# Kernel tuning notes

Hardware: AMD Instinct MI355X
Metric: run time of the kernel (lower is better)

The kernel has to match this reference:

```python
import jax, jax.numpy as jnp
import numpy as np

B, S, D, H, HH, L = 256, 512, 128, 256, 128, 64
PATH_V, SYS_V = 10000, 500

def _gru_cell(gi_t, h, Whh, bhh):
    # PyTorch GRU cell: gi_t = x @ Wih.T + bih precomputed
    gh = h @ Whh.T + bhh
    ir, iz, inn = jnp.split(gi_t, 3, axis=-1)
    hr, hz, hn = jnp.split(gh, 3, axis=-1)
    r = jax.nn.sigmoid(ir + hr)
    z = jax.nn.sigmoid(iz + hz)
    n = jnp.tanh(inn + r * hn)
    return (1.0 - z) * n + z * h

def _gru_seq(x, Wih, Whh, bih, bhh):
    # x: [B,S,in] -> outputs [B,S,H], zero initial hidden (torch default)
    gi = jnp.einsum('bsd,hd->bsh', x, Wih) + bih  # precompute input gates once
    h0 = jnp.zeros((x.shape[0], Whh.shape[1]), x.dtype)
    def step(h, gi_t):
        hn = _gru_cell(gi_t, h, Whh, bhh)
        return hn, hn
    _, ys = jax.lax.scan(step, h0, jnp.swapaxes(gi, 0, 1))
    return jnp.swapaxes(ys, 0, 1)

def setup_inputs() -> dict:
    key = jax.random.key(0)
    ks = jax.random.split(key, 24)
    r = lambda k, shape: (jax.random.normal(k, shape, dtype=jnp.float32) * 0.05)
    inp = {
        'tokens': jax.random.randint(ks[0], (B, S, 2), 0, SYS_V, dtype=jnp.int64),
        'path_emb_w': r(ks[1], (PATH_V, D)),
        'sys_emb_w': r(ks[2], (SYS_V, D)),
        # encoder gru1: D -> H
        'e1_Wih': r(ks[3], (3 * H, D)), 'e1_Whh': r(ks[4], (3 * H, H)),
        'e1_bih': r(ks[5], (3 * H,)), 'e1_bhh': r(ks[6], (3 * H,)),
        # encoder gru2: H -> HH
        'e2_Wih': r(ks[7], (3 * HH, H)), 'e2_Whh': r(ks[8], (3 * HH, HH)),
        'e2_bih': r(ks[9], (3 * HH,)), 'e2_bhh': r(ks[10], (3 * HH,)),
        # linear1: HH -> L
        'l1_W': r(ks[11], (L, HH)), 'l1_b': r(ks[12], (L,)),
        # decoder gru1: L -> HH
        'd1_Wih': r(ks[13], (3 * HH, L)), 'd1_Whh': r(ks[14], (3 * HH, HH)),
        'd1_bih': r(ks[15], (3 * HH,)), 'd1_bhh': r(ks[16], (3 * HH,)),
        # decoder gru2: HH -> H
        'd2_Wih': r(ks[17], (3 * H, HH)), 'd2_Whh': r(ks[18], (3 * H, H)),
        'd2_bih': r(ks[19], (3 * H,)), 'd2_bhh': r(ks[20], (3 * H,)),
        # linear2: H -> D
        'l2_W': r(ks[21], (D, H)), 'l2_b': r(ks[22], (D,)),
    }
    return inp

def reference(tokens, path_emb_w, sys_emb_w,
              e1_Wih, e1_Whh, e1_bih, e1_bhh,
              e2_Wih, e2_Whh, e2_bih, e2_bhh,
              l1_W, l1_b,
              d1_Wih, d1_Whh, d1_bih, d1_bhh,
              d2_Wih, d2_Whh, d2_bih, d2_bhh,
              l2_W, l2_b):
    # embedding sum -> [B,S,D]
    emb = path_emb_w[tokens[:, :, 0]] + sys_emb_w[tokens[:, :, 1]]
    # encoder (dropout is identity at eval)
    h1_seq = _gru_seq(emb, e1_Wih, e1_Whh, e1_bih, e1_bhh)      # [B,S,H]
    h2_seq = _gru_seq(h1_seq, e2_Wih, e2_Whh, e2_bih, e2_bhh)    # [B,S,HH]
    latent = h2_seq[:, -1, :] @ l1_W.T + l1_b                    # [B,L]
    gi1 = latent @ d1_Wih.T + d1_bih                             # constant [B,3*HH]
    h10 = jnp.zeros((latent.shape[0], HH), latent.dtype)
    h20 = jnp.zeros((latent.shape[0], H), latent.dtype)
    def dec_step(carry, _):
        h1, h2 = carry
        h1 = _gru_cell(gi1, h1, d1_Whh, d1_bhh)
        gi2 = h1 @ d2_Wih.T + d2_bih
        h2 = _gru_cell(gi2, h2, d2_Whh, d2_bhh)
        out = h2 @ l2_W.T + l2_b                                 # linear2 per step
        return (h1, h2), out
    _, outs = jax.lax.scan(dec_step, (h10, h20), None, length=S)  # [S,B,D]
    recon = jnp.swapaxes(outs, 0, 1)                             # [B,S,D]
    recon_loss = jnp.mean((recon - emb) ** 2)
    return latent, recon_loss
```

## Files before the change

### kernel.cpp

```cpp
#include <hip/hip_runtime.h>
#include <cstddef>

typedef unsigned short u16;
typedef __bf16 bf16x8 __attribute__((ext_vector_type(8)));
typedef float f32x4 __attribute__((ext_vector_type(4)));
typedef unsigned short us4 __attribute__((ext_vector_type(4)));

__device__ __forceinline__ u16 f2b(float f) {
    unsigned u = __float_as_uint(f);
    u += 0x7fffu + ((u >> 16) & 1u);
    return (u16)(u >> 16);
}
__device__ __forceinline__ float b2f(u16 h) { return __uint_as_float(((unsigned)h) << 16); }

__device__ __forceinline__ f32x4 mfma16(bf16x8 a, bf16x8 b, f32x4 c) {
    return __builtin_amdgcn_mfma_f32_16x16x32_bf16(a, b, c, 0, 0, 0);
}

__device__ __forceinline__ void bar_lds() {
    asm volatile("s_waitcnt lgkmcnt(0)\n\ts_barrier" ::: "memory");
}

#define CH   64
#define NCH  8
#define MCH  (CH * 256)

struct PackSeg { const float* src; u16* dst; int K; int nfrag; };
struct PackArgs { PackSeg seg[8]; };

__global__ __launch_bounds__(64) void pack_all(PackArgs pa) {
    int f = blockIdx.x;
    int i = 0;
    while (i < 7 && f >= pa.seg[i].nfrag) { f -= pa.seg[i].nfrag; i++; }
    const float* W = pa.seg[i].src;
    u16* out = pa.seg[i].dst;
    int K = pa.seg[i].K;
    int lane = threadIdx.x, q = lane >> 4, ln = lane & 15;
    int KT = K >> 5;
    int nt = f / KT, kt = f % KT;
    int n = nt * 16 + ln;
    int kb = kt * 32 + q * 8;
#pragma unroll
    for (int j = 0; j < 8; j++)
        out[((size_t)f * 64 + lane) * 8 + j] = f2b(W[(size_t)n * K + kb + j]);
}

__global__ void zero_kernel(float* __restrict__ st, float* __restrict__ lossslot) {
    int i = blockIdx.x * 256 + threadIdx.x;
    if (i < 196608) st[i] = 0.f;
    if (i == 0) *lossslot = 0.f;
}

__global__ __launch_bounds__(256) void embed_kernel(const int* __restrict__ tok,
                                                    const float* __restrict__ pw,
                                                    const float* __restrict__ sw,
                                                    u16* __restrict__ emb) {
    int col = threadIdx.x & 127;
    int half = threadIdx.x >> 7;
    int rbase = blockIdx.x * 16;
#pragma unroll
    for (int i = 0; i < 8; i++) {
        int r = rbase + i * 2 + half;
        int b = r & 255, t = r >> 8;
        const int* tp = tok + ((size_t)b * 512 + t) * 2;
        float v = pw[(size_t)tp[0] * 128 + col] + sw[(size_t)tp[1] * 128 + col];
        emb[(size_t)r * 128 + col] = f2b(v);
    }
}

template <int K, int N>
__device__ __forceinline__ void gemm_body(int bid, char* ldsraw,
                                          const u16* __restrict__ X,
                                          const u16* __restrict__ Wp,
                                          const float* __restrict__ bias,
                                          const float* __restrict__ bhh,
                                          u16* __restrict__ out) {
    constexpr int NH = N / 2, KT = K / 32, NTL = NH / 16;
    u16* wl = (u16*)ldsraw;
    int tid = threadIdx.x, wid = tid >> 6, lane = tid & 63, q = lane >> 4, ln = lane & 15;
    int half = bid & 1, mg = bid >> 1;
    {
        const bf16x8* src = (const bf16x8*)(Wp + (size_t)half * NH * K);
        bf16x8* dst = (bf16x8*)wl;
#pragma unroll
        for (int i = 0; i < NH * K / 8 / 512; i++) dst[tid + i * 512] = src[tid + i * 512];
    }
    __syncthreads();
    int m0 = (mg * 8 + wid) * 16;
    int t = m0 >> 8, bg = (m0 >> 4) & 15;
    u16* obase = out + (size_t)(t * 16 + bg) * N * 16;
    bf16x8 af[KT];
#pragma unroll
    for (int kt = 0; kt < KT; kt++)
        af[kt] = *(const bf16x8*)(X + (size_t)(m0 + ln) * K + kt * 32 + q * 8);
    for (int nt = 0; nt < NTL; nt++) {
        f32x4 acc = {0.f, 0.f, 0.f, 0.f};
#pragma unroll
        for (int kt = 0; kt < KT; kt++)
            acc = mfma16(af[kt], *(const bf16x8*)&wl[((nt * KT + kt) * 64 + lane) * 8], acc);
        int g = half * NH + nt * 16 + ln;
        float bv = bias[g] + ((g < 2 * (N / 3)) ? bhh[g] : 0.f);
        us4 v;
#pragma unroll
        for (int r = 0; r < 4; r++) v[r] = f2b(acc[r] + bv);
        *(us4*)&obase[(size_t)g * 16 + 4 * q] = v;
    }
}

template <int K, int N>
__global__ __launch_bounds__(512, 2) void gemm_kernel(const u16* __restrict__ X,
                                                      const u16* __restrict__ Wp,
                                                      const float* __restrict__ bias,
                                                      const float* __restrict__ bhh,
                                                      u16* __restrict__ out) {
    __shared__ char lds[98304];
    gemm_body<K, N>(blockIdx.x, lds, X, Wp, bias, bhh, out);
}

__device__ __forceinline__ void loss_body(int bid, char* ldsraw,
                                          const u16* __restrict__ h2d,
                                          const u16* __restrict__ Wp,
                                          const float* __restrict__ l2b,
                                          const u16* __restrict__ embc,
                                          float* __restrict__ loss) {
    float* red = (float*)ldsraw;
    int tid = threadIdx.x, wid = tid >> 6, lane = tid & 63, q = lane >> 4, ln = lane & 15;
    int m0 = (bid * 8 + wid) * 16;
    bf16x8 af[8];
#pragma unroll
    for (int kt = 0; kt < 8; kt++)
        af[kt] = *(const bf16x8*)(h2d + (size_t)(m0 + ln) * 256 + kt * 32 + q * 8);
    float ls = 0.f;
#pragma unroll
    for (int nt = 0; nt < 8; nt++) {
        f32x4 acc = {0.f, 0.f, 0.f, 0.f};
#pragma unroll
        for (int kt = 0; kt < 8; kt++)
            acc = mfma16(af[kt], *(const bf16x8*)(Wp + ((size_t)(nt * 8 + kt) * 64 + lane) * 8), acc);
        int g = nt * 16 + ln;
        float bv = l2b[g];
#pragma unroll
        for (int r = 0; r < 4; r++) {
            float rec = acc[r] + bv;
            float ev = b2f(embc[(size_t)(m0 + q * 4 + r) * 128 + g]);
            float d = rec - ev;
            ls += d * d;
        }
    }
    red[tid] = ls;
    __syncthreads();
    for (int s = 256; s > 0; s >>= 1) {
        if (tid < s) red[tid] += red[tid + s];
        __syncthreads();
    }
    if (tid == 0) atomicAdd(loss, red[0] * (1.f / 16777216.f));
}

template <int H, bool GI_CONST, bool WRITE_SEQ>
__device__ __forceinline__ void rec_body(int bid, char* ldsraw,
                                         const u16* __restrict__ giT,
                                         const float* __restrict__ gic,
                                         const u16* __restrict__ Wp,
                                         const float* __restrict__ bhh,
                                         float* __restrict__ hstate,
                                         u16* __restrict__ hseq, int steps) {
    constexpr int G3 = 3 * H;
    constexpr int KT = H / 32;
    constexpr int NHF = H / 128;
    constexpr int HP = H + 8;
    constexpr bool WLDS = (H == 256);
    u16* wl = (u16*)ldsraw;
    u16 (*hl)[16][HP] = (u16 (*)[16][HP])(ldsraw + (WLDS ? 65536 : 0));

    const int tid = threadIdx.x, w = tid >> 6, lane = tid & 63, q = lane >> 4, ln = lane & 15;
    const int b0 = bid * 16;
    const bf16x8* wpv = (const bf16x8*)Wp;

    bf16x8 wfr[3][NHF][KT];
#pragma unroll
    for (int g = 0; g < 3; g++)
#pragma unroll
        for (int hh = 0; hh < NHF; hh++) {
            if (WLDS && g == 2 && hh == NHF - 1) continue;
#pragma unroll
            for (int kt = 0; kt < KT; kt++)
                wfr[g][hh][kt] = wpv[((size_t)(g * (H / 16) + NHF * w + hh) * KT + kt) * 64 + lane];
        }
    if (WLDS) {
#pragma unroll
        for (int kt = 0; kt < KT; kt++)
            *(bf16x8*)&wl[((w * KT + kt) * 64 + lane) * 8] =
                wpv[((size_t)(2 * (H / 16) + NHF * w + (NHF - 1)) * KT + kt) * 64 + lane];
    }
    float bhn_r[NHF];
#pragma unroll
    for (int hh = 0; hh < NHF; hh++) bhn_r[hh] = bhh[2 * H + 16 * (NHF * w + hh) + ln];

    float hold[NHF][4];
#pragma unroll
    for (int hh = 0; hh < NHF; hh++)
#pragma unroll
        for (int rg = 0; rg < 4; rg++) {
            const int b = 4 * q + rg, k = 16 * (NHF * w + hh) + ln;
            u16 hb = f2b(hstate[(size_t)(b0 + b) * H + k]);
            hold[hh][rg] = b2f(hb);
            hl[0][b][k] = hb;
        }

    float gcf[3][NHF][4];
    us4 gp[3][NHF];
    if (GI_CONST) {
#pragma unroll
        for (int g = 0; g < 3; g++)
#pragma unroll
            for (int hh = 0; hh < NHF; hh++)
#pragma unroll
                for (int rg = 0; rg < 4; rg++)
                    gcf[g][hh][rg] =
                        gic[(size_t)(b0 + 4 * q + rg) * G3 + g * H + 16 * (NHF * w + hh) + ln];
    } else {
        const u16* blk = giT + (size_t)bid * G3 * 16;
#pragma unroll
        for (int g = 0; g < 3; g++)
#pragma unroll
            for (int hh = 0; hh < NHF; hh++)
                gp[g][hh] = *(const us4*)&blk[(g * H + 16 * (NHF * w + hh) + ln) * 16 + 4 * q];
    }
    bar_lds();

    for (int t = 0; t < steps; t++) {
        const int p = t & 1;
        float gf2[NHF][4];
        f32x4 acc[3][NHF];
#pragma unroll
        for (int hh = 0; hh < NHF; hh++) {
#pragma unroll
            for (int rg = 0; rg < 4; rg++) {
                if (GI_CONST) {
                    acc[0][hh][rg] = gcf[0][hh][rg];
                    acc[1][hh][rg] = gcf[1][hh][rg];
                    gf2[hh][rg] = gcf[2][hh][rg];
                } else {
                    acc[0][hh][rg] = b2f(gp[0][hh][rg]);
                    acc[1][hh][rg] = b2f(gp[1][hh][rg]);
                    gf2[hh][rg] = b2f(gp[2][hh][rg]);
                }
                acc[2][hh][rg] = bhn_r[hh];
            }
        }
        if (!GI_CONST) {
            const int tn = (t + 1 < steps) ? t + 1 : t;
            const u16* blk = giT + (size_t)(tn * 16 + bid) * G3 * 16;
#pragma unroll
            for (int g = 0; g < 3; g++)
#pragma unroll
                for (int hh = 0; hh < NHF; hh++)
                    gp[g][hh] = *(const us4*)&blk[(g * H + 16 * (NHF * w + hh) + ln) * 16 + 4 * q];
        }

        u16* hsb = WRITE_SEQ ? (hseq + ((size_t)t * 256 + b0) * H) : nullptr;

#pragma unroll
        for (int hh = 0; hh < NHF; hh++) {
            const int k = 16 * (NHF * w + hh) + ln;
#pragma unroll
            for (int kh = 0; kh < KT / 2; kh++) {
                bf16x8 a0 = *(const bf16x8*)&hl[p][ln][(2 * kh) * 32 + q * 8];
                bf16x8 a1 = *(const bf16x8*)&hl[p][ln][(2 * kh + 1) * 32 + q * 8];
                acc[0][hh] = mfma16(a0, wfr[0][hh][2 * kh], acc[0][hh]);
                acc[0][hh] = mfma16(a1, wfr[0][hh][2 * kh + 1], acc[0][hh]);
                acc[1][hh] = mfma16(a0, wfr[1][hh][2 * kh], acc[1][hh]);
                acc[1][hh] = mfma16(a1, wfr[1][hh][2 * kh + 1], acc[1][hh]);
                if (WLDS && hh == NHF - 1) {
                    bf16x8 w0 = *(const bf16x8*)&wl[((w * KT + 2 * kh) * 64 + lane) * 8];
                    bf16x8 w1 = *(const bf16x8*)&wl[((w * KT + 2 * kh + 1) * 64 + lane) * 8];
                    acc[2][hh] = mfma16(a0, w0, acc[2][hh]);
                    acc[2][hh] = mfma16(a1, w1, acc[2][hh]);
                } else {
                    acc[2][hh] = mfma16(a0, wfr[2][hh][2 * kh], acc[2][hh]);
                    acc[2][hh] = mfma16(a1, wfr[2][hh][2 * kh + 1], acc[2][hh]);
                }
            }
#pragma unroll
            for (int rg = 0; rg < 4; rg++) {
                float xr = acc[0][hh][rg];
                float xz = acc[1][hh][rg];
                float hn = acc[2][hh][rg];
                float r = __builtin_amdgcn_rcpf(1.f + __builtin_amdgcn_exp2f(-1.44269504f * xr));
                float z = __builtin_amdgcn_rcpf(1.f + __builtin_amdgcn_exp2f(-1.44269504f * xz));
                float y = gf2[hh][rg] + r * hn;
                float e2 = __builtin_amdgcn_exp2f(2.88539008f * y);
                float n = 1.f - 2.f * __builtin_amdgcn_rcpf(e2 + 1.f);
                float hv = n + z * (hold[hh][rg] - n);
                u16 hb = f2b(hv);
                hold[hh][rg] = b2f(hb);
                hl[p ^ 1][4 * q + rg][k] = hb;
                if (WRITE_SEQ) hsb[(size_t)(4 * q + rg) * H + k] = hb;
            }
        }
        bar_lds();
    }
#pragma unroll
    for (int hh = 0; hh < NHF; hh++)
#pragma unroll
        for (int rg = 0; rg < 4; rg++)
            hstate[(size_t)(b0 + 4 * q + rg) * H + 16 * (NHF * w + hh) + ln] = hold[hh][rg];
}

__global__ __launch_bounds__(512, 2) void enc_pair(
    int nb1, int nb2, int ng1,
    const u16* r1gi, const u16* r1W, const float* r1bhh, float* r1st, u16* r1seq,
    const u16* r2gi, const u16* r2W, const float* r2bhh, float* r2st,
    const u16* g1X, const u16* g1W, const float* g1b, const float* g1bhh, u16* g1out,
    const u16* g2X, const u16* g2W, const float* g2b, const float* g2bhh, u16* g2out,
    int steps) {
    __shared__ char lds[98304];
    int b = blockIdx.x;
    if (b < nb1)
        rec_body<256, false, true>(b, lds, r1gi, nullptr, r1W, r1bhh, r1st, r1seq, steps);
    else if (b < nb1 + nb2)
        rec_body<128, false, false>(b - nb1, lds, r2gi, nullptr, r2W, r2bhh, r2st, nullptr, steps);
    else if (b < nb1 + nb2 + ng1)
        gemm_body<128, 768>(b - nb1 - nb2, lds, g1X, g1W, g1b, g1bhh, g1out);
    else
        gemm_body<256, 384>(b - nb1 - nb2 - ng1, lds, g2X, g2W, g2b, g2bhh, g2out);
}

__global__ __launch_bounds__(512, 2) void dec_pair(
    int nb1, int nb2, int ng,
    const float* r1gic, const u16* r1W, const float* r1bhh, float* r1st, u16* r1seq,
    const u16* r2gi, const u16* r2W, const float* r2bhh, float* r2st, u16* r2seq,
    const u16* gX, const u16* gW, const float* gb, const float* gbhh, u16* gout,
    const u16* lh2, const u16* lW, const float* l2b, const u16* lemb, float* lloss,
    int steps) {
    __shared__ char lds[98304];
    int b = blockIdx.x;
    if (b < nb1)
        rec_body<128, true, true>(b, lds, nullptr, r1gic, r1W, r1bhh, r1st, r1seq, steps);
    else if (b < nb1 + nb2)
        rec_body<256, false, true>(b - nb1, lds, r2gi, nullptr, r2W, r2bhh, r2st, r2seq, steps);
    else if (b < nb1 + nb2 + ng)
        gemm_body<128, 768>(b - nb1 - nb2, lds, gX, gW, gb, gbhh, gout);
    else
        loss_body(b - nb1 - nb2 - ng, lds, lh2, lW, l2b, lemb, lloss);
}

__global__ __launch_bounds__(128) void latent_kernel(const float* __restrict__ st2,
                                                     const float* __restrict__ l1W,
                                                     const float* __restrict__ l1b,
                                                     const float* __restrict__ d1Wih,
                                                     const float* __restrict__ d1bih,
                                                     const float* __restrict__ d1bhh,
                                                     float* __restrict__ dout,
                                                     float* __restrict__ gi1dec) {
    __shared__ float hv[128], lat[64];
    int b = blockIdx.x, tid = threadIdx.x;
    hv[tid] = st2[(size_t)b * 128 + tid];
    __syncthreads();
    if (tid < 64) {
        float s = l1b[tid];
        for (int k = 0; k < 128; k++) s += l1W[tid * 128 + k] * hv[k];
        dout[b * 64 + tid] = s;
        lat[tid] = s;
    }
    __syncthreads();
    for (int g = tid; g < 384; g += 128) {
        float s = d1bih[g] + (g < 256 ? d1bhh[g] : 0.f);
        for (int k = 0; k < 64; k++) s += d1Wih[g * 64 + k] * lat[k];
        gi1dec[(size_t)b * 384 + g] = s;
    }
}

extern "C" void kernel_launch(void* const* d_in, const int* in_sizes, int n_in,
                              void* d_out, int out_size, void* d_ws, size_t ws_size,
                              hipStream_t stream) {
    (void)in_sizes; (void)n_in; (void)out_size; (void)ws_size;
    const int*   tok   = (const int*)d_in[0];
    const float* pw    = (const float*)d_in[1];
    const float* sw    = (const float*)d_in[2];
    const float* e1Wih = (const float*)d_in[3];
    const float* e1Whh = (const float*)d_in[4];
    const float* e1bih = (const float*)d_in[5];
    const float* e1bhh = (const float*)d_in[6];
    const float* e2Wih = (const float*)d_in[7];
    const float* e2Whh = (const float*)d_in[8];
    const float* e2bih = (const float*)d_in[9];
    const float* e2bhh = (const float*)d_in[10];
    const float* l1W   = (const float*)d_in[11];
    const float* l1b   = (const float*)d_in[12];
    const float* d1Wih = (const float*)d_in[13];
    const float* d1Whh = (const float*)d_in[14];
    const float* d1bih = (const float*)d_in[15];
    const float* d1bhh = (const float*)d_in[16];
    const float* d2Wih = (const float*)d_in[17];
    const float* d2Whh = (const float*)d_in[18];
    const float* d2bih = (const float*)d_in[19];
    const float* d2bhh = (const float*)d_in[20];
    const float* l2W   = (const float*)d_in[21];
    const float* l2b   = (const float*)d_in[22];
    float* dout = (float*)d_out;

    char* base = (char*)d_ws;
    size_t o = 0;
    auto alloc = [&](size_t bytes) { size_t r = o; o += (bytes + 255) & ~(size_t)255; return r; };
    u16* e1Wih_p = (u16*)(base + alloc(196608));
    u16* e1Whh_p = (u16*)(base + alloc(393216));
    u16* e2Wih_p = (u16*)(base + alloc(196608));
    u16* e2Whh_p = (u16*)(base + alloc(98304));
    u16* d1Whh_p = (u16*)(base + alloc(98304));
    u16* d2Wih_p = (u16*)(base + alloc(196608));
    u16* d2Whh_p = (u16*)(base + alloc(393216));
    u16* l2W_p   = (u16*)(base + alloc(65536));
    u16* emb_p   = (u16*)(base + alloc((size_t)131072 * 128 * 2));
    u16* giA0    = (u16*)(base + alloc((size_t)MCH * 768 * 2));
    u16* giA1    = (u16*)(base + alloc((size_t)MCH * 768 * 2));
    u16* giB0    = (u16*)(base + alloc((size_t)MCH * 384 * 2));
    u16* giB1    = (u16*)(base + alloc((size_t)MCH * 384 * 2));
    u16* h1c0    = (u16*)(base + alloc((size_t)MCH * 256 * 2));
    u16* h1c1    = (u16*)(base + alloc((size_t)MCH * 256 * 2));
    u16* h2c0    = (u16*)(base + alloc((size_t)MCH * 256 * 2));
    u16* h2c1    = (u16*)(base + alloc((size_t)MCH * 256 * 2));
    float* st1 = (float*)(base + alloc(256 * 256 * 4));
    float* st2 = (float*)(base + alloc(256 * 128 * 4));
    float* st3 = (float*)(base + alloc(256 * 128 * 4));
    float* st4 = (float*)(base + alloc(256 * 256 * 4));
    float* gi1dec = (float*)(base + alloc(256 * 384 * 4));
    u16* giA[2] = {giA0, giA1};
    u16* giB[2] = {giB0, giB1};
    u16* h1c[2] = {h1c0, h1c1};
    u16* h2c[2] = {h2c0, h2c1};

    PackArgs pa;
    pa.seg[0] = {e1Wih, e1Wih_p, 128, 192};
    pa.seg[1] = {e1Whh, e1Whh_p, 256, 384};
    pa.seg[2] = {e2Wih, e2Wih_p, 256, 192};
    pa.seg[3] = {e2Whh, e2Whh_p, 128, 96};
    pa.seg[4] = {d1Whh, d1Whh_p, 128, 96};
    pa.seg[5] = {d2Wih, d2Wih_p, 128, 192};
    pa.seg[6] = {d2Whh, d2Whh_p, 256, 384};
    pa.seg[7] = {l2W,   l2W_p,   256, 64};
    pack_all<<<1600, 64, 0, stream>>>(pa);
    zero_kernel<<<769, 256, 0, stream>>>(st1, dout + 16384);
    embed_kernel<<<8192, 256, 0, stream>>>(tok, pw, sw, emb_p);

    gemm_kernel<128, 768><<<256, 512, 0, stream>>>(emb_p, e1Wih_p, e1bih, e1bhh, giA[0]);
    for (int c = 0; c < NCH; c++) {
        int nb2 = (c >= 2) ? 16 : 0;
        int ng1 = (c <= 6) ? 256 : 0;
        int ng2 = (c >= 1) ? 256 : 0;
        enc_pair<<<16 + nb2 + ng1 + ng2, 512, 0, stream>>>(16, nb2, ng1,
            giA[c & 1], e1Whh_p, e1bhh, st1, h1c[c & 1],
            giB[(c - 2) & 1], e2Whh_p, e2bhh, st2,
            emb_p + (size_t)((c + 1) & 7) * MCH * 128, e1Wih_p, e1bih, e1bhh, giA[(c + 1) & 1],
            h1c[(c - 1) & 1], e2Wih_p, e2bih, e2bhh, giB[(c - 1) & 1], CH);
    }
    enc_pair<<<16 + 256, 512, 0, stream>>>(0, 16, 0,
        giA[0], e1Whh_p, e1bhh, st1, h1c[0],
        giB[0], e2Whh_p, e2bhh, st2,
        emb_p, e1Wih_p, e1bih, e1bhh, giA[0],
        h1c[1], e2Wih_p, e2bih, e2bhh, giB[1], CH);
    enc_pair<<<16, 512, 0, stream>>>(0, 16, 0,
        giA[0], e1Whh_p, e1bhh, st1, h1c[0],
        giB[1], e2Whh_p, e2bhh, st2,
        emb_p, e1Wih_p, e1bih, e1bhh, giA[0],
        h1c[0], e2Wih_p, e2bih, e2bhh, giB[0], CH);

    latent_kernel<<<256, 128, 0, stream>>>(st2, l1W, l1b, d1Wih, d1bih, d1bhh, dout, gi1dec);

    for (int c = 0; c <= 10; c++) {
        int nb1 = (c <= 7) ? 16 : 0;
        int ng  = (c >= 1 && c <= 8) ? 256 : 0;
        int nb2 = (c >= 2 && c <= 9) ? 16 : 0;
        int nl  = (c >= 3) ? 128 : 0;
        dec_pair<<<nb1 + nb2 + ng + nl, 512, 0, stream>>>(nb1, nb2, ng,
            gi1dec, d1Whh_p, d1bhh, st3, h1c[c & 1],
            giA[(c - 2) & 1], d2Whh_p, d2bhh, st4, h2c[(c - 2) & 1],
            h1c[(c - 1) & 1], d2Wih_p, d2bih, d2bhh, giA[(c - 1) & 1],
            h2c[(c - 3) & 1], l2W_p, l2b, emb_p + (size_t)((c - 3) & 7) * MCH * 128,
            dout + 16384, CH);
    }
}
```

Before: 2.178 ms.

## Halve pipeline chunk size and hoist all-gate MFMA loop before activations

Cuts the time-chunk length from 64 to 32 steps (16 chunks), so the pipelined encoder and decoder stages fill and drain faster. Grid sizes for the GEMM, projection and linear blocks are halved to match. The recurrent step now issues every MFMA for all gates and hidden fragments before any activation math, which gives the matrix core more independent work to overlap. The cost is twice as many kernel launches and more live accumulator registers.

```diff
diff --git a/kernel.cpp b/kernel.cpp
--- a/kernel.cpp
+++ b/kernel.cpp
@@ -21,8 +21,8 @@
     asm volatile("s_waitcnt lgkmcnt(0)\n\ts_barrier" ::: "memory");
 }
 
-#define CH   64
-#define NCH  8
+#define CH   32
+#define NCH  16
 #define MCH  (CH * 256)
 
 struct PackSeg { const float* src; u16* dst; int K; int nfrag; };
@@ -258,29 +258,30 @@
                     gp[g][hh] = *(const us4*)&blk[(g * H + 16 * (NHF * w + hh) + ln) * 16 + 4 * q];
         }
 
+#pragma unroll
+        for (int kh = 0; kh < KT / 2; kh++) {
+            bf16x8 a0 = *(const bf16x8*)&hl[p][ln][(2 * kh) * 32 + q * 8];
+            bf16x8 a1 = *(const bf16x8*)&hl[p][ln][(2 * kh + 1) * 32 + q * 8];
+#pragma unroll
+            for (int g = 0; g < 3; g++)
+#pragma unroll
+                for (int hh = 0; hh < NHF; hh++) {
+                    if (WLDS && g == 2 && hh == NHF - 1) {
+                        bf16x8 w0 = *(const bf16x8*)&wl[((w * KT + 2 * kh) * 64 + lane) * 8];
+                        bf16x8 w1 = *(const bf16x8*)&wl[((w * KT + 2 * kh + 1) * 64 + lane) * 8];
+                        acc[g][hh] = mfma16(a0, w0, acc[g][hh]);
+                        acc[g][hh] = mfma16(a1, w1, acc[g][hh]);
+                    } else {
+                        acc[g][hh] = mfma16(a0, wfr[g][hh][2 * kh], acc[g][hh]);
+                        acc[g][hh] = mfma16(a1, wfr[g][hh][2 * kh + 1], acc[g][hh]);
+                    }
+                }
+        }
+
         u16* hsb = WRITE_SEQ ? (hseq + ((size_t)t * 256 + b0) * H) : nullptr;
-
 #pragma unroll
         for (int hh = 0; hh < NHF; hh++) {
             const int k = 16 * (NHF * w + hh) + ln;
-#pragma unroll
-            for (int kh = 0; kh < KT / 2; kh++) {
-                bf16x8 a0 = *(const bf16x8*)&hl[p][ln][(2 * kh) * 32 + q * 8];
-                bf16x8 a1 = *(const bf16x8*)&hl[p][ln][(2 * kh + 1) * 32 + q * 8];
-                acc[0][hh] = mfma16(a0, wfr[0][hh][2 * kh], acc[0][hh]);
-                acc[0][hh] = mfma16(a1, wfr[0][hh][2 * kh + 1], acc[0][hh]);
-                acc[1][hh] = mfma16(a0, wfr[1][hh][2 * kh], acc[1][hh]);
-                acc[1][hh] = mfma16(a1, wfr[1][hh][2 * kh + 1], acc[1][hh]);
-                if (WLDS && hh == NHF - 1) {
-                    bf16x8 w0 = *(const bf16x8*)&wl[((w * KT + 2 * kh) * 64 + lane) * 8];
-                    bf16x8 w1 = *(const bf16x8*)&wl[((w * KT + 2 * kh + 1) * 64 + lane) * 8];
-                    acc[2][hh] = mfma16(a0, w0, acc[2][hh]);
-                    acc[2][hh] = mfma16(a1, w1, acc[2][hh]);
-                } else {
-                    acc[2][hh] = mfma16(a0, wfr[2][hh][2 * kh], acc[2][hh]);
-                    acc[2][hh] = mfma16(a1, wfr[2][hh][2 * kh + 1], acc[2][hh]);
-                }
-            }
 #pragma unroll
             for (int rg = 0; rg < 4; rg++) {
                 float xr = acc[0][hh][rg];
@@ -443,40 +444,41 @@
     zero_kernel<<<769, 256, 0, stream>>>(st1, dout + 16384);
     embed_kernel<<<8192, 256, 0, stream>>>(tok, pw, sw, emb_p);
 
-    gemm_kernel<128, 768><<<256, 512, 0, stream>>>(emb_p, e1Wih_p, e1bih, e1bhh, giA[0]);
+    gemm_kernel<128, 768><<<128, 512, 0, stream>>>(emb_p, e1Wih_p, e1bih, e1bhh, giA[0]);
     for (int c = 0; c < NCH; c++) {
         int nb2 = (c >= 2) ? 16 : 0;
-        int ng1 = (c <= 6) ? 256 : 0;
-        int ng2 = (c >= 1) ? 256 : 0;
+        int ng1 = (c <= NCH - 2) ? 128 : 0;
+        int ng2 = (c >= 1) ? 128 : 0;
         enc_pair<<<16 + nb2 + ng1 + ng2, 512, 0, stream>>>(16, nb2, ng1,
             giA[c & 1], e1Whh_p, e1bhh, st1, h1c[c & 1],
             giB[(c - 2) & 1], e2Whh_p, e2bhh, st2,
-            emb_p + (size_t)((c + 1) & 7) * MCH * 128, e1Wih_p, e1bih, e1bhh, giA[(c + 1) & 1],
+            emb_p + (size_t)((c + 1) & (NCH - 1)) * MCH * 128, e1Wih_p, e1bih, e1bhh,
+            giA[(c + 1) & 1],
             h1c[(c - 1) & 1], e2Wih_p, e2bih, e2bhh, giB[(c - 1) & 1], CH);
     }
-    enc_pair<<<16 + 256, 512, 0, stream>>>(0, 16, 0,
+    enc_pair<<<16 + 128, 512, 0, stream>>>(0, 16, 0,
         giA[0], e1Whh_p, e1bhh, st1, h1c[0],
-        giB[0], e2Whh_p, e2bhh, st2,
+        giB[(NCH - 2) & 1], e2Whh_p, e2bhh, st2,
         emb_p, e1Wih_p, e1bih, e1bhh, giA[0],
-        h1c[1], e2Wih_p, e2bih, e2bhh, giB[1], CH);
+        h1c[(NCH - 1) & 1], e2Wih_p, e2bih, e2bhh, giB[(NCH - 1) & 1], CH);
     enc_pair<<<16, 512, 0, stream>>>(0, 16, 0,
         giA[0], e1Whh_p, e1bhh, st1, h1c[0],
-        giB[1], e2Whh_p, e2bhh, st2,
+        giB[(NCH - 1) & 1], e2Whh_p, e2bhh, st2,
         emb_p, e1Wih_p, e1bih, e1bhh, giA[0],
         h1c[0], e2Wih_p, e2bih, e2bhh, giB[0], CH);
 
     latent_kernel<<<256, 128, 0, stream>>>(st2, l1W, l1b, d1Wih, d1bih, d1bhh, dout, gi1dec);
 
-    for (int c = 0; c <= 10; c++) {
-        int nb1 = (c <= 7) ? 16 : 0;
-        int ng  = (c >= 1 && c <= 8) ? 256 : 0;
-        int nb2 = (c >= 2 && c <= 9) ? 16 : 0;
-        int nl  = (c >= 3) ? 128 : 0;
+    for (int c = 0; c <= NCH + 2; c++) {
+        int nb1 = (c <= NCH - 1) ? 16 : 0;
+        int ng  = (c >= 1 && c <= NCH) ? 128 : 0;
+        int nb2 = (c >= 2 && c <= NCH + 1) ? 16 : 0;
+        int nl  = (c >= 3) ? 64 : 0;
         dec_pair<<<nb1 + nb2 + ng + nl, 512, 0, stream>>>(nb1, nb2, ng,
             gi1dec, d1Whh_p, d1bhh, st3, h1c[c & 1],
             giA[(c - 2) & 1], d2Whh_p, d2bhh, st4, h2c[(c - 2) & 1],
             h1c[(c - 1) & 1], d2Wih_p, d2bih, d2bhh, giA[(c - 1) & 1],
-            h2c[(c - 3) & 1], l2W_p, l2b, emb_p + (size_t)((c - 3) & 7) * MCH * 128,
+            h2c[(c - 3) & 1], l2W_p, l2b, emb_p + (size_t)((c - 3) & (NCH - 1)) * MCH * 128,
             dout + 16384, CH);
     }
 }
```

After: 1.901 ms, median of 2. 1.15x faster.
